# Performance work log

Measured on AMD Instinct MI355X. Metric: run time of the kernel, lower is better.

## Reference

```python
import jax, jax.numpy as jnp
import numpy as np

B, D_IN, HD, HN = 16384, 1024, 128, 8
D = HD * HN  # 1024
PROJ = int((4.0 / 3.0) * D)  # 1365
EPS = 1e-5


def setup_inputs() -> dict:
    key = jax.random.key(0)
    ks = jax.random.split(key, 16)
    s = 0.02
    inp = {
        'seq': jax.random.normal(ks[0], (B, D_IN), jnp.float32),
        'c0': jnp.zeros((B, D), jnp.float32),
        'n0': jnp.ones((B, D), jnp.float32),
        'h0': jax.random.normal(ks[1], (B, D), jnp.float32) * 0.1,
        'm0': jnp.zeros((B, D), jnp.float32),
        'ln_w': jnp.ones((D_IN,), jnp.float32),
        'ln_b': jnp.zeros((D_IN,), jnp.float32),
        'Wz': jax.random.normal(ks[2], (D, D_IN), jnp.float32) * s,
        'bz': jnp.zeros((D,), jnp.float32),
        'Wi': jax.random.normal(ks[3], (D, D_IN), jnp.float32) * s,
        'bi': jnp.zeros((D,), jnp.float32),
        'Wo': jax.random.normal(ks[4], (D, D_IN), jnp.float32) * s,
        'bo': jnp.zeros((D,), jnp.float32),
        'Wf': jax.random.normal(ks[5], (D, D_IN), jnp.float32) * s,
        'bf': jnp.zeros((D,), jnp.float32),
        'Rz': jax.random.normal(ks[6], (HN, HD, HD), jnp.float32) * s,
        'Ri': jax.random.normal(ks[7], (HN, HD, HD), jnp.float32) * s,
        'Ro': jax.random.normal(ks[8], (HN, HD, HD), jnp.float32) * s,
        'Rf': jax.random.normal(ks[9], (HN, HD, HD), jnp.float32) * s,
        'gn_w': jnp.ones((D,), jnp.float32),
        'gn_b': jnp.zeros((D,), jnp.float32),
        'up_w': jax.random.normal(ks[10], (2 * PROJ, D), jnp.float32) * s,
        'up_b': jnp.zeros((2 * PROJ,), jnp.float32),
        'down_w': jax.random.normal(ks[11], (D_IN, PROJ), jnp.float32) * s,
        'down_b': jnp.zeros((D_IN,), jnp.float32),
    }
    return inp


def _layernorm(x, w, b):
    mu = jnp.mean(x, axis=-1, keepdims=True)
    var = jnp.mean(jnp.square(x - mu), axis=-1, keepdims=True)
    return (x - mu) * jax.lax.rsqrt(var + EPS) * w + b


def _groupnorm(x, w, b):
    # x: (B, D) -> groups of HD channels per head
    xr = x.reshape(x.shape[0], HN, HD)
    mu = jnp.mean(xr, axis=-1, keepdims=True)
    var = jnp.mean(jnp.square(xr - mu), axis=-1, keepdims=True)
    xn = ((xr - mu) * jax.lax.rsqrt(var + EPS)).reshape(x.shape)
    return xn * w + b


def _block_linear(h, R):
    # block-diagonal recurrence: per-head (HD,HD) matmul
    hr = h.reshape(h.shape[0], HN, HD)
    return jnp.einsum('hed,bhd->bhe', R, hr).reshape(h.shape)


def reference(seq, c0, n0, h0, m0, ln_w, ln_b, Wz, bz, Wi, bi, Wo, bo, Wf, bf,
              Rz, Ri, Ro, Rf, gn_w, gn_b, up_w, up_b, down_w, down_b):
    x_t = _layernorm(seq, ln_w, ln_b)
    x_c = x_t  # use_conv=False default path
    i_t = x_c @ Wi.T + bi + _block_linear(h0, Ri)
    f_t = x_c @ Wf.T + bf + _block_linear(h0, Rf)
    z_t = x_t @ Wz.T + bz + _block_linear(h0, Rz)
    o_t = x_t @ Wo.T + bo + _block_linear(h0, Ro)
    m_t = jnp.maximum(f_t + m0, i_t)
    i_e = jnp.exp(i_t - m_t)
    f_e = jnp.exp(f_t - m_t + m0)
    z_a = jnp.tanh(z_t)
    o_a = jax.nn.sigmoid(o_t)
    c_t = f_e * c0 + i_e * z_a
    n_t = f_e * n0 + i_e
    h_t = o_a * (c_t / n_t)
    out = _groupnorm(h_t, gn_w, gn_b)
    up = out @ up_w.T + up_b
    out1, out2 = jnp.split(up, 2, axis=-1)
    out = out1 + jax.nn.gelu(out2, approximate=False)
    out = out @ down_w.T + down_b
    return (out + seq, c_t, n_t, h_t, m_t)
```

## Files before the change

### kernel.cpp

```cpp
#include <hip/hip_runtime.h>
#include <hip/hip_bf16.h>
#include <cstdint>
#include <type_traits>

typedef __attribute__((ext_vector_type(8))) __bf16 bf16x8;
typedef __attribute__((ext_vector_type(8))) short short8;
typedef __attribute__((ext_vector_type(4))) float f32x4;
using u16 = unsigned short;

template <typename T, typename = void> struct mfma_ok : std::false_type {};
template <typename T>
struct mfma_ok<T, std::void_t<decltype(__builtin_amdgcn_mfma_f32_16x16x32_bf16(
    std::declval<T>(), std::declval<T>(), std::declval<f32x4>(), 0, 0, 0))>>
    : std::true_type {};
using frag_t = std::conditional_t<mfma_ok<bf16x8>::value, bf16x8, short8>;
static_assert(sizeof(frag_t) == 16, "frag must be 4 VGPRs");

template <typename T>
__device__ __forceinline__ f32x4 MFMA(T a, T b, f32x4 c) {
  return __builtin_amdgcn_mfma_f32_16x16x32_bf16(a, b, c, 0, 0, 0);
}

__device__ __forceinline__ void gl_lds16(const u16* g, u16* l) {
  __builtin_amdgcn_global_load_lds(
      (const __attribute__((address_space(1))) unsigned int*)g,
      (__attribute__((address_space(3))) unsigned int*)l, 16, 0, 0);
}

__device__ __forceinline__ u16 f2bf(float v) {
  __hip_bfloat16 h = __float2bfloat16(v);
  return __builtin_bit_cast(u16, h);
}

__device__ __forceinline__ int xcd_swz(int wid, int nwg) {
  return (wid & 7) * (nwg >> 3) + (wid >> 3);
}

__device__ __forceinline__ void gemm256(
    const u16* __restrict__ A, int lda,
    const u16* __restrict__ B, int ldb, int K,
    u16* lds, f32x4 (&acc)[8][4])
{
  const int t = threadIdx.x;
  const int l = t & 63;
  const int w = t >> 6;
  const int wm = w >> 2, wc = w & 3;

  const int srow = t >> 2;
  const int skc = (t & 3) ^ ((srow & 3) ^ ((srow >> 2) & 3));
  const u16* gA0 = A + srow * lda + skc * 8;
  const u16* gB0 = B + srow * ldb + skc * 8;
  const u16* gA1 = gA0 + 128 * lda;
  const u16* gB1 = gB0 + 128 * ldb;

  const int dA0 = w * 512, dA1 = 4096 + w * 512;
  const int dB0 = 8192 + w * 512, dB1 = 12288 + w * 512;

  u16* s0 = lds;
  u16* s1 = lds + 16384;
  u16* s2 = lds + 32768;

  const int kcA = (l >> 4) ^ (l & 3) ^ ((l >> 2) & 3);
  const int aBase = (wm * 128 + (l & 15)) * 32 + kcA * 8;
  const int bBase = 8192 + (wc * 64 + (l & 15)) * 32 + kcA * 8;

  const int nt = K >> 5;

#define STAGE_TILE(slot, kt) do {                 \
    const int ko_ = (kt) * 32;                    \
    gl_lds16(gA0 + ko_, (slot) + dA0);            \
    gl_lds16(gA1 + ko_, (slot) + dA1);            \
    gl_lds16(gB0 + ko_, (slot) + dB0);            \
    gl_lds16(gB1 + ko_, (slot) + dB1);            \
  } while (0)

  STAGE_TILE(s0, 0);
  STAGE_TILE(s1, 1);
  asm volatile("s_waitcnt vmcnt(4)" ::: "memory");
  __builtin_amdgcn_s_barrier();
  __builtin_amdgcn_sched_barrier(0);

  for (int kt = 0; kt < nt; ++kt) {
    const bool more = (kt + 2 < nt);
    if (more) STAGE_TILE(s2, kt + 2);
    frag_t a[8];
#pragma unroll
    for (int fm = 0; fm < 8; ++fm)
      a[fm] = *(const frag_t*)(s0 + aBase + fm * 512);
    __builtin_amdgcn_s_setprio(1);
#pragma unroll
    for (int fn = 0; fn < 4; ++fn) {
      frag_t b = *(const frag_t*)(s0 + bBase + fn * 512);
#pragma unroll
      for (int fm = 0; fm < 8; ++fm)
        acc[fm][fn] = MFMA(a[fm], b, acc[fm][fn]);
    }
    __builtin_amdgcn_s_setprio(0);
    if (more) asm volatile("s_waitcnt vmcnt(4)" ::: "memory");
    else      asm volatile("s_waitcnt vmcnt(0)" ::: "memory");
    __builtin_amdgcn_s_barrier();
    __builtin_amdgcn_sched_barrier(0);
    u16* tmp = s0; s0 = s1; s1 = s2; s2 = tmp;
  }
#undef STAGE_TILE
}

__global__ __launch_bounds__(256) void prep_kernel(
    const float* __restrict__ Wi, const float* __restrict__ Wf,
    const float* __restrict__ Wz, const float* __restrict__ Wo,
    const float* __restrict__ Ri, const float* __restrict__ Rf,
    const float* __restrict__ Rz, const float* __restrict__ Ro,
    const float* __restrict__ upw, const float* __restrict__ dnw,
    u16* __restrict__ Wint, u16* __restrict__ Rint,
    u16* __restrict__ upint, u16* __restrict__ dnp)
{
  const int stride = gridDim.x * 256;
  for (int i = blockIdx.x * 256 + threadIdx.x; i < 9043968; i += stride) {
    if (i < 4194304) {
      const int s = i >> 18, v = (i >> 10) & 255, k = i & 1023;
      const int wc = v >> 6, gsel = (v >> 4) & 3, c16 = v & 15;
      const int srcRow = s * 64 + wc * 16 + c16;
      const float* W = (gsel == 0) ? Wi : (gsel == 1) ? Wf : (gsel == 2) ? Wz : Wo;
      Wint[i] = f2bf(W[srcRow * 1024 + k]);
    } else if (i < 4718592) {
      const int j = i - 4194304;
      const int s = j >> 15, v = (j >> 7) & 255, k = j & 127;
      const int wc = v >> 6, gsel = (v >> 4) & 3, c16 = v & 15;
      const int head = s >> 1;
      const int colInHead = (s & 1) * 64 + wc * 16 + c16;
      const float* R = (gsel == 0) ? Ri : (gsel == 1) ? Rf : (gsel == 2) ? Rz : Ro;
      Rint[j] = f2bf(R[head * 16384 + colInHead * 128 + k]);
    } else if (i < 7602176) {
      const int j = i - 4718592;
      const int vcol = j >> 10, k = j & 1023;
      const int tile = vcol >> 8, wc = (vcol >> 6) & 3;
      const int half = (vcol >> 5) & 1, c32 = vcol & 31;
      const int a = tile * 128 + wc * 32 + c32;
      upint[j] = (a < 1365) ? f2bf(upw[(half * 1365 + a) * 1024 + k]) : (u16)0;
    } else {
      const int j = i - 7602176;
      const int row = j / 1408, k = j - row * 1408;
      dnp[j] = (k < 1365) ? f2bf(dnw[row * 1365 + k]) : (u16)0;
    }
  }
}

__global__ __launch_bounds__(256) void ln_kernel(
    const float* __restrict__ seq, const float* __restrict__ h0,
    const float* __restrict__ lnw, const float* __restrict__ lnb,
    u16* __restrict__ xb, u16* __restrict__ h0b)
{
  const int row = blockIdx.x;
  const int t = threadIdx.x;
  const float4 v = ((const float4*)(seq + (size_t)row * 1024))[t];
  float s = v.x + v.y + v.z + v.w;
  float q = v.x * v.x + v.y * v.y + v.z * v.z + v.w * v.w;
#pragma unroll
  for (int o = 32; o >= 1; o >>= 1) { s += __shfl_xor(s, o); q += __shfl_xor(q, o); }
  __shared__ float sm[8];
  const int l = t & 63, w = t >> 6;
  if (l == 0) { sm[w] = s; sm[4 + w] = q; }
  __syncthreads();
  s = sm[0] + sm[1] + sm[2] + sm[3];
  q = sm[4] + sm[5] + sm[6] + sm[7];
  const float mu = s * (1.f / 1024.f);
  const float var = q * (1.f / 1024.f) - mu * mu;
  const float rstd = rsqrtf(var + 1e-5f);
  const float4 wv = ((const float4*)lnw)[t];
  const float4 bv = ((const float4*)lnb)[t];
  ushort4 o4;
  o4.x = f2bf((v.x - mu) * rstd * wv.x + bv.x);
  o4.y = f2bf((v.y - mu) * rstd * wv.y + bv.y);
  o4.z = f2bf((v.z - mu) * rstd * wv.z + bv.z);
  o4.w = f2bf((v.w - mu) * rstd * wv.w + bv.w);
  ((ushort4*)(xb + (size_t)row * 1024))[t] = o4;
  const float4 h = ((const float4*)(h0 + (size_t)row * 1024))[t];
  ushort4 h4;
  h4.x = f2bf(h.x); h4.y = f2bf(h.y); h4.z = f2bf(h.z); h4.w = f2bf(h.w);
  ((ushort4*)(h0b + (size_t)row * 1024))[t] = h4;
}

__global__ __launch_bounds__(512, 2) void gate_kernel(
    const u16* __restrict__ xb, const u16* __restrict__ h0b,
    const u16* __restrict__ Wint, const u16* __restrict__ Rint,
    const float* __restrict__ bi, const float* __restrict__ bfv,
    const float* __restrict__ bz, const float* __restrict__ bo,
    const float* __restrict__ c0, const float* __restrict__ n0i,
    const float* __restrict__ m0,
    float* __restrict__ oc, float* __restrict__ on,
    float* __restrict__ oh, float* __restrict__ om)
{
  __shared__ __align__(16) u16 lds[49152];
  const int wid = xcd_swz(blockIdx.x, 1024);
  const int s = wid & 15;
  const int m0r = (wid >> 4) * 256;
  f32x4 acc[8][4] = {};
  gemm256(xb + (size_t)m0r * 1024, 1024, Wint + s * 262144, 1024, 1024, lds, acc);
  const int head = s >> 1;
  gemm256(h0b + (size_t)m0r * 1024 + head * 128, 1024,
          Rint + s * 32768, 128, 128, lds, acc);

  const int t = threadIdx.x, l = t & 63, w = t >> 6, wm = w >> 2, wc = w & 3;
  const int cc = s * 64 + wc * 16 + (l & 15);
  const float biv = bi[cc], bfvv = bfv[cc], bzv = bz[cc], bov = bo[cc];
#pragma unroll
  for (int fm = 0; fm < 8; ++fm) {
    const int rbase = m0r + wm * 128 + fm * 16 + (l >> 4) * 4;
#pragma unroll
    for (int r = 0; r < 4; ++r) {
      const size_t idx = (size_t)(rbase + r) * 1024 + cc;
      const float it = acc[fm][0][r] + biv;
      const float ft = acc[fm][1][r] + bfvv;
      const float zt = acc[fm][2][r] + bzv;
      const float ot = acc[fm][3][r] + bov;
      const float mp = m0[idx];
      const float mt = fmaxf(ft + mp, it);
      const float ie = __expf(it - mt);
      const float fe = __expf(ft - mt + mp);
      const float ct = fe * c0[idx] + ie * tanhf(zt);
      const float nt = fe * n0i[idx] + ie;
      const float ht = (ct / nt) / (1.f + __expf(-ot));
      oc[idx] = ct; on[idx] = nt; oh[idx] = ht; om[idx] = mt;
    }
  }
}

__global__ __launch_bounds__(256) void gn_kernel(
    const float* __restrict__ h, const float* __restrict__ gw,
    const float* __restrict__ gb, u16* __restrict__ gnb)
{
  const int t = threadIdx.x, l = t & 63, w = t >> 6;
  for (int grp = blockIdx.x * 4 + w; grp < 16384 * 8; grp += gridDim.x * 4) {
    const int b = grp >> 3, hd = grp & 7;
    const float2 v = ((const float2*)(h + b * 1024 + hd * 128))[l];
    float s = v.x + v.y, q = v.x * v.x + v.y * v.y;
#pragma unroll
    for (int o = 32; o >= 1; o >>= 1) { s += __shfl_xor(s, o); q += __shfl_xor(q, o); }
    const float mu = s * (1.f / 128.f);
    const float var = q * (1.f / 128.f) - mu * mu;
    const float rstd = rsqrtf(var + 1e-5f);
    const float2 wv = ((const float2*)(gw + hd * 128))[l];
    const float2 bv = ((const float2*)(gb + hd * 128))[l];
    ushort2 o2;
    o2.x = f2bf((v.x - mu) * rstd * wv.x + bv.x);
    o2.y = f2bf((v.y - mu) * rstd * wv.y + bv.y);
    ((ushort2*)(gnb + b * 1024 + hd * 128))[l] = o2;
  }
}

__global__ __launch_bounds__(512, 2) void up_kernel(
    const u16* __restrict__ gnb, const u16* __restrict__ upint,
    const float* __restrict__ upb, u16* __restrict__ g)
{
  __shared__ __align__(16) u16 lds[49152];
  const int wid = xcd_swz(blockIdx.x, 704);
  const int vt = wid % 11, mt = wid / 11;
  const int m0r = mt * 256;
  f32x4 acc[8][4] = {};
  gemm256(gnb + (size_t)m0r * 1024, 1024, upint + vt * 262144, 1024, 1024,
          lds, acc);
  const int t = threadIdx.x, l = t & 63, w = t >> 6, wm = w >> 2, wc = w & 3;
#pragma unroll
  for (int fm = 0; fm < 8; ++fm) {
    const int rbase = m0r + wm * 128 + fm * 16 + (l >> 4) * 4;
#pragma unroll
    for (int fn = 0; fn < 2; ++fn) {
      const int a = vt * 128 + wc * 32 + fn * 16 + (l & 15);
      const float b1 = (a < 1365) ? upb[a] : 0.f;
      const float b2 = (a < 1365) ? upb[1365 + a] : 0.f;
#pragma unroll
      for (int r = 0; r < 4; ++r) {
        const float u1 = acc[fm][fn][r] + b1;
        const float u2 = acc[fm][fn + 2][r] + b2;
        const float ge = 0.5f * u2 * (1.f + erff(u2 * 0.70710678118654752f));
        g[(size_t)(rbase + r) * 1408 + a] = f2bf(u1 + ge);
      }
    }
  }
}

__global__ __launch_bounds__(512, 2) void down_kernel(
    const u16* __restrict__ g, const u16* __restrict__ dnp,
    const float* __restrict__ dnb, const float* __restrict__ seq,
    float* __restrict__ out)
{
  __shared__ __align__(16) u16 lds[49152];
  const int wid = xcd_swz(blockIdx.x, 256);
  const int nc = (wid & 3) * 256;
  const int m0r = (wid >> 2) * 256;
  f32x4 acc[8][4] = {};
  gemm256(g + (size_t)m0r * 1408, 1408, dnp + nc * 1408, 1408, 1408, lds, acc);
  const int t = threadIdx.x, l = t & 63, w = t >> 6, wm = w >> 2, wc = w & 3;
#pragma unroll
  for (int fm = 0; fm < 8; ++fm) {
    const int rbase = m0r + wm * 128 + fm * 16 + (l >> 4) * 4;
#pragma unroll
    for (int fn = 0; fn < 4; ++fn) {
      const int cc = nc + wc * 64 + fn * 16 + (l & 15);
      const float bb = dnb[cc];
#pragma unroll
      for (int r = 0; r < 4; ++r) {
        const size_t idx = (size_t)(rbase + r) * 1024 + cc;
        out[idx] = acc[fm][fn][r] + bb + seq[idx];
      }
    }
  }
}

extern "C" void kernel_launch(void* const* d_in, const int* in_sizes, int n_in,
                              void* d_out, int out_size, void* d_ws, size_t ws_size,
                              hipStream_t stream) {
  const float* seq = (const float*)d_in[0];
  const float* c0  = (const float*)d_in[1];
  const float* n0i = (const float*)d_in[2];
  const float* h0  = (const float*)d_in[3];
  const float* m0  = (const float*)d_in[4];
  const float* lnw = (const float*)d_in[5];
  const float* lnb = (const float*)d_in[6];
  const float* Wz  = (const float*)d_in[7];
  const float* bz  = (const float*)d_in[8];
  const float* Wi  = (const float*)d_in[9];
  const float* bi  = (const float*)d_in[10];
  const float* Wo  = (const float*)d_in[11];
  const float* bo  = (const float*)d_in[12];
  const float* Wf  = (const float*)d_in[13];
  const float* bf_ = (const float*)d_in[14];
  const float* Rz  = (const float*)d_in[15];
  const float* Ri  = (const float*)d_in[16];
  const float* Ro  = (const float*)d_in[17];
  const float* Rf  = (const float*)d_in[18];
  const float* gw  = (const float*)d_in[19];
  const float* gb  = (const float*)d_in[20];
  const float* upw = (const float*)d_in[21];
  const float* upb = (const float*)d_in[22];
  const float* dnw = (const float*)d_in[23];
  const float* dnb = (const float*)d_in[24];

  char* ws = (char*)d_ws;
  u16* xb   = (u16*)(ws);
  u16* h0b  = (u16*)(ws + 33554432);
  u16* Wint = (u16*)(ws + 67108864);
  u16* Rint = (u16*)(ws + 75497472);
  u16* upc  = (u16*)(ws + 76546048);
  u16* dnp  = (u16*)(ws + 82313216);
  u16* g    = (u16*)(ws + 85196800);

  float* out = (float*)d_out;
  float* oc = out + 16777216;
  float* on = out + 2 * 16777216;
  float* oh = out + 3 * 16777216;
  float* om = out + 4 * 16777216;

  prep_kernel<<<dim3(2048), dim3(256), 0, stream>>>(
      Wi, Wf, Wz, Wo, Ri, Rf, Rz, Ro, upw, dnw, Wint, Rint, upc, dnp);
  ln_kernel<<<dim3(16384), dim3(256), 0, stream>>>(seq, h0, lnw, lnb, xb, h0b);
  gate_kernel<<<dim3(1024), dim3(512), 0, stream>>>(
      xb, h0b, Wint, Rint, bi, bf_, bz, bo, c0, n0i, m0, oc, on, oh, om);
  gn_kernel<<<dim3(2048), dim3(256), 0, stream>>>(oh, gw, gb, xb);
  up_kernel<<<dim3(704), dim3(512), 0, stream>>>(xb, upc, upb, g);
  down_kernel<<<dim3(256), dim3(512), 0, stream>>>(g, dnp, dnb, seq, out);
}
```

Measured before the change: 533.8 us.

## Widen GEMM K-tile to 64 and switch to double-buffered LDS staging

The shared gemm256 routine now stages 64-wide K slices instead of 32, with an XOR swizzle over 8 chunks. The three-slot LDS ring is replaced by two 64 KB buffers, and each stage is fully drained with vmcnt(0) before the barrier. Each iteration issues two sub-steps of 32 MFMAs with A and B fragments preloaded, so there are half as many barriers and loop iterations per K. The trade-off is shallower prefetch: only one tile is in flight instead of two. LDS per block also grows to 128 KB in the gate, up and down kernels.

```diff
diff --git a/kernel.cpp b/kernel.cpp
--- a/kernel.cpp
+++ b/kernel.cpp
@@ -46,63 +46,65 @@
   const int w = t >> 6;
   const int wm = w >> 2, wc = w & 3;
 
-  const int srow = t >> 2;
-  const int skc = (t & 3) ^ ((srow & 3) ^ ((srow >> 2) & 3));
-  const u16* gA0 = A + srow * lda + skc * 8;
-  const u16* gB0 = B + srow * ldb + skc * 8;
-  const u16* gA1 = gA0 + 128 * lda;
-  const u16* gB1 = gB0 + 128 * ldb;
-
-  const int dA0 = w * 512, dA1 = 4096 + w * 512;
-  const int dB0 = 8192 + w * 512, dB1 = 12288 + w * 512;
-
-  u16* s0 = lds;
-  u16* s1 = lds + 16384;
-  u16* s2 = lds + 32768;
-
-  const int kcA = (l >> 4) ^ (l & 3) ^ ((l >> 2) & 3);
-  const int aBase = (wm * 128 + (l & 15)) * 32 + kcA * 8;
-  const int bBase = 8192 + (wc * 64 + (l & 15)) * 32 + kcA * 8;
-
-  const int nt = K >> 5;
-
-#define STAGE_TILE(slot, kt) do {                 \
-    const int ko_ = (kt) * 32;                    \
-    gl_lds16(gA0 + ko_, (slot) + dA0);            \
-    gl_lds16(gA1 + ko_, (slot) + dA1);            \
-    gl_lds16(gB0 + ko_, (slot) + dB0);            \
-    gl_lds16(gB1 + ko_, (slot) + dB1);            \
+  const int sc = (t & 7) ^ ((t >> 3) & 7);
+  const u16* gA = A + (t >> 3) * lda + sc * 8;
+  const u16* gB = B + (t >> 3) * ldb + sc * 8;
+
+#define STAGE(buf, kt) do {                                   \
+    const u16* a_ = gA + (kt) * 64;                           \
+    const u16* b_ = gB + (kt) * 64;                           \
+    u16* s_ = (buf);                                          \
+    gl_lds16(a_,             s_ + w * 512);                   \
+    gl_lds16(a_ +  64 * lda, s_ +  4096 + w * 512);           \
+    gl_lds16(a_ + 128 * lda, s_ +  8192 + w * 512);           \
+    gl_lds16(a_ + 192 * lda, s_ + 12288 + w * 512);           \
+    gl_lds16(b_,             s_ + 16384 + w * 512);           \
+    gl_lds16(b_ +  64 * ldb, s_ + 20480 + w * 512);           \
+    gl_lds16(b_ + 128 * ldb, s_ + 24576 + w * 512);           \
+    gl_lds16(b_ + 192 * ldb, s_ + 28672 + w * 512);           \
   } while (0)
 
-  STAGE_TILE(s0, 0);
-  STAGE_TILE(s1, 1);
-  asm volatile("s_waitcnt vmcnt(4)" ::: "memory");
+  const int lr = l & 15;
+  const int lk = l >> 4;
+  const int lx = l & 7;
+  const int pk0 = ((0 + lk) ^ lx) * 8;
+  const int pk1 = ((4 + lk) ^ lx) * 8;
+  const int arow0 = (wm * 128 + lr) * 64;
+  const int brow0 = 16384 + (wc * 64 + lr) * 64;
+
+  const int nt = K >> 6;
+
+  STAGE(lds, 0);
+  asm volatile("s_waitcnt vmcnt(0)" ::: "memory");
   __builtin_amdgcn_s_barrier();
-  __builtin_amdgcn_sched_barrier(0);
 
   for (int kt = 0; kt < nt; ++kt) {
-    const bool more = (kt + 2 < nt);
-    if (more) STAGE_TILE(s2, kt + 2);
-    frag_t a[8];
-#pragma unroll
-    for (int fm = 0; fm < 8; ++fm)
-      a[fm] = *(const frag_t*)(s0 + aBase + fm * 512);
-    __builtin_amdgcn_s_setprio(1);
-#pragma unroll
-    for (int fn = 0; fn < 4; ++fn) {
-      frag_t b = *(const frag_t*)(s0 + bBase + fn * 512);
+    u16* cur = lds + (kt & 1) * 32768;
+    u16* nxt = lds + ((kt + 1) & 1) * 32768;
+    if (kt + 1 < nt) STAGE(nxt, kt + 1);
+    __builtin_amdgcn_sched_barrier(0);
+#pragma unroll
+    for (int kf = 0; kf < 2; ++kf) {
+      const int pk = kf ? pk1 : pk0;
+      frag_t a[8], b[4];
 #pragma unroll
       for (int fm = 0; fm < 8; ++fm)
-        acc[fm][fn] = MFMA(a[fm], b, acc[fm][fn]);
-    }
-    __builtin_amdgcn_s_setprio(0);
-    if (more) asm volatile("s_waitcnt vmcnt(4)" ::: "memory");
-    else      asm volatile("s_waitcnt vmcnt(0)" ::: "memory");
+        a[fm] = *(const frag_t*)(cur + arow0 + fm * 1024 + pk);
+#pragma unroll
+      for (int fn = 0; fn < 4; ++fn)
+        b[fn] = *(const frag_t*)(cur + brow0 + fn * 1024 + pk);
+      __builtin_amdgcn_s_setprio(1);
+#pragma unroll
+      for (int fn = 0; fn < 4; ++fn)
+#pragma unroll
+        for (int fm = 0; fm < 8; ++fm)
+          acc[fm][fn] = MFMA(a[fm], b[fn], acc[fm][fn]);
+      __builtin_amdgcn_s_setprio(0);
+    }
+    asm volatile("s_waitcnt vmcnt(0)" ::: "memory");
     __builtin_amdgcn_s_barrier();
-    __builtin_amdgcn_sched_barrier(0);
-    u16* tmp = s0; s0 = s1; s1 = s2; s2 = tmp;
-  }
-#undef STAGE_TILE
+  }
+#undef STAGE
 }
 
 __global__ __launch_bounds__(256) void prep_kernel(
@@ -190,7 +192,7 @@
     float* __restrict__ oc, float* __restrict__ on,
     float* __restrict__ oh, float* __restrict__ om)
 {
-  __shared__ __align__(16) u16 lds[49152];
+  __shared__ __align__(16) u16 lds[65536];
   const int wid = xcd_swz(blockIdx.x, 1024);
   const int s = wid & 15;
   const int m0r = (wid >> 4) * 256;
@@ -252,7 +254,7 @@
     const u16* __restrict__ gnb, const u16* __restrict__ upint,
     const float* __restrict__ upb, u16* __restrict__ g)
 {
-  __shared__ __align__(16) u16 lds[49152];
+  __shared__ __align__(16) u16 lds[65536];
   const int wid = xcd_swz(blockIdx.x, 704);
   const int vt = wid % 11, mt = wid / 11;
   const int m0r = mt * 256;
@@ -284,7 +286,7 @@
     const float* __restrict__ dnb, const float* __restrict__ seq,
     float* __restrict__ out)
 {
-  __shared__ __align__(16) u16 lds[49152];
+  __shared__ __align__(16) u16 lds[65536];
   const int wid = xcd_swz(blockIdx.x, 256);
   const int nc = (wid & 3) * 256;
   const int m0r = (wid >> 2) * 256;
```

Result: faster. 505.9 us (-5.2%).
